# Optimization experiments

Measured on AMD Instinct MI355X. Metric: run time of the kernel, lower is better.

## Reference

```python
import jax, jax.numpy as jnp
import numpy as np

B, S, DIM, NH = 2, 2048, 1536, 12
HD = DIM // NH            # 128
C = HD // 2               # 64 rotary pairs
CF = C - 2 * (C // 3)     # 22 (frame axis)
CH = C // 3               # 21 (height axis)
CW = C // 3               # 21 (width axis)
GF, GH, GW = 8, 16, 16    # grid sizes, GF*GH*GW == S
EPS = 1e-6


def _freq_table(n_pos, dim):
    inv = 1.0 / (10000.0 ** (np.arange(dim, dtype=np.float64) / dim))
    ang = np.outer(np.arange(n_pos, dtype=np.float64), inv)
    return (np.cos(ang).astype(np.float32), np.sin(ang).astype(np.float32))


def setup_inputs() -> dict:
    key = jax.random.key(0)
    ks = jax.random.split(key, 8)
    scale = 0.02
    cos_f, sin_f = _freq_table(GF, CF)
    cos_h, sin_h = _freq_table(GH, CH)
    cos_w, sin_w = _freq_table(GW, CW)
    return {
        'x': jax.random.normal(ks[0], (B, S, DIM), dtype=jnp.float32),
        'seq_lens': jnp.array([2048, 1600], dtype=jnp.int32),
        'f': GF, 'h': GH, 'w': GW,
        'wq': scale * jax.random.normal(ks[1], (DIM, DIM), dtype=jnp.float32),
        'bq': jnp.zeros((DIM,), jnp.float32),
        'wk': scale * jax.random.normal(ks[2], (DIM, DIM), dtype=jnp.float32),
        'bk': jnp.zeros((DIM,), jnp.float32),
        'wv': scale * jax.random.normal(ks[3], (DIM, DIM), dtype=jnp.float32),
        'bv': jnp.zeros((DIM,), jnp.float32),
        'wo': scale * jax.random.normal(ks[4], (DIM, DIM), dtype=jnp.float32),
        'bo': jnp.zeros((DIM,), jnp.float32),
        'nq_w': jnp.ones((DIM,), jnp.float32),
        'nk_w': jnp.ones((DIM,), jnp.float32),
        'cos_f': jnp.asarray(cos_f), 'sin_f': jnp.asarray(sin_f),
        'cos_h': jnp.asarray(cos_h), 'sin_h': jnp.asarray(sin_h),
        'cos_w': jnp.asarray(cos_w), 'sin_w': jnp.asarray(sin_w),
    }


def _rmsnorm(t, wt):
    return t * jax.lax.rsqrt(jnp.mean(t * t, axis=-1, keepdims=True) + EPS) * wt


def _grid_rope(t, cos, sin, b, s):
    # t: [b, s, NH, HD] ; cos/sin: [s, 1, C] (per-position assembled freqs)
    tp = t.reshape(b, s, NH, C, 2)
    xr, xi = tp[..., 0], tp[..., 1]
    rr = xr * cos - xi * sin          # complex multiply by e^{i*theta}
    ri = xr * sin + xi * cos
    return jnp.stack([rr, ri], axis=-1).reshape(b, s, NH, HD)


def reference(x, seq_lens, f, h, w, wq, bq, wk, bk, wv, bv, wo, bo,
              nq_w, nk_w, cos_f, sin_f, cos_h, sin_h, cos_w, sin_w):
    b, s, _ = x.shape
    # QKV projections with RMSNorm on q/k over full dim (as in the module)
    q = _rmsnorm(x @ wq.T + bq, nq_w).reshape(b, s, NH, HD)
    k = _rmsnorm(x @ wk.T + bk, nk_w).reshape(b, s, NH, HD)
    v = (x @ wv.T + bv).reshape(b, s, NH, HD)
    # grid-indexed RoPE: zero offsets / target==grid => arange sampling per axis
    idx = jnp.arange(s)
    fi = idx // (h * w)
    hi = (idx // w) % h
    wi = idx % w
    cos = jnp.concatenate([cos_f[fi], cos_h[hi], cos_w[wi]], axis=-1)[:, None, :]
    sin = jnp.concatenate([sin_f[fi], sin_h[hi], sin_w[wi]], axis=-1)[:, None, :]
    qr = _grid_rope(q, cos, sin, b, s)
    kr = _grid_rope(k, cos, sin, b, s)
    # attention with ragged key-length masking (flash_attention k_lens)
    scale = 1.0 / jnp.sqrt(jnp.float32(HD))
    scores = jnp.einsum('bqnd,bknd->bnqk', qr, kr) * scale
    kmask = idx[None, :] < seq_lens[:, None]            # [b, s]
    scores = jnp.where(kmask[:, None, None, :], scores, jnp.float32(-1e30))
    attn = jax.nn.softmax(scores, axis=-1)
    out = jnp.einsum('bnqk,bknd->bqnd', attn, v).reshape(b, s, DIM)
    return out @ wo.T + bo
```

## Files before the change

kernel.cpp:

```cpp
#include <hip/hip_runtime.h>
#include <hip/hip_bf16.h>
#include <math.h>

#define DIM_  1536
#define NH_   12
#define HD_   128
#define S_    2048
#define B_    2
#define M_    (B_*S_)
#define WEL_  (DIM_*DIM_)

typedef __attribute__((ext_vector_type(8))) _Float16 f16x8;
typedef __attribute__((ext_vector_type(4))) short short4v;
typedef __attribute__((ext_vector_type(8))) short short8v;
typedef __attribute__((ext_vector_type(4))) float f32x4;

#define SSCALE_LOG2E (0.08838834764831845f * 1.4426950408889634f)

static __device__ __forceinline__ short f2h(float f) {
  union { _Float16 h; short s; } u;
  u.h = (_Float16)f;
  return u.s;
}

static __device__ __forceinline__ unsigned pk2h(float a, float b) {
  typedef __attribute__((ext_vector_type(2))) __fp16 fp16x2;
  union { fp16x2 v; unsigned u; } u2;
  u2.v = __builtin_amdgcn_cvt_pkrtz(a, b);
  return u2.u;
}

__global__ __launch_bounds__(256) void f2h5_k(
    const float* __restrict__ x, const float* __restrict__ wq,
    const float* __restrict__ wk, const float* __restrict__ wv,
    const float* __restrict__ wo,
    short* __restrict__ x16, short* __restrict__ w16, short* __restrict__ wo16)
{
  int i = blockIdx.x * 256 + threadIdx.x;
  const float* src; short* dst; int j;
  if (i < 786432)       { src = x;  dst = x16;            j = i; }
  else if (i < 1081344) { src = wq; dst = w16;            j = i - 786432; }
  else if (i < 1376256) { src = wk; dst = w16 + WEL_;     j = i - 1081344; }
  else if (i < 1671168) { src = wv; dst = w16 + 2 * WEL_; j = i - 1376256; }
  else                  { src = wo; dst = wo16;           j = i - 1671168; }
  const float4* p = (const float4*)src + (size_t)j * 2;
  float4 a = p[0], b = p[1];
  short8v o;
  o[0] = f2h(a.x); o[1] = f2h(a.y); o[2] = f2h(a.z); o[3] = f2h(a.w);
  o[4] = f2h(b.x); o[5] = f2h(b.y); o[6] = f2h(b.z); o[7] = f2h(b.w);
  *((short8v*)dst + j) = o;
}

template<int MODE>
static __device__ __forceinline__ void gemm16_core(
    const short* __restrict__ A16, const short* __restrict__ W16,
    const float* __restrict__ bias, short* __restrict__ Outp,
    int m0, int n0, char* __restrict__ Ab, char* __restrict__ Bb)
{
  const int tid = threadIdx.x;
  const int l  = tid & 63, w = tid >> 6;
  const int wr = w >> 1, wc = w & 1;
  const int lc = l & 15, lg = l >> 4;

  f32x4 acc[4][4] = {};

  const int rs  = w * 16 + (l >> 2);
  const int gsl = ((l & 3) ^ ((rs >> 1) & 3)) * 8;
  const short* gA0 = A16 + (size_t)(m0 + rs) * DIM_ + gsl;
  const short* gA1 = A16 + (size_t)(m0 + 64 + rs) * DIM_ + gsl;
  const short* gB0 = W16 + (size_t)(n0 + rs) * DIM_ + gsl;
  const short* gB1 = W16 + (size_t)(n0 + 64 + rs) * DIM_ + gsl;

#define GSTAGE(buf, k0)                                                        \
  {                                                                            \
    __builtin_amdgcn_global_load_lds(                                          \
        (const __attribute__((address_space(1))) unsigned*)(gA0 + (k0)),       \
        (__attribute__((address_space(3))) unsigned*)(Ab + (buf) * 8192 + w * 1024), 16, 0, 0); \
    __builtin_amdgcn_global_load_lds(                                          \
        (const __attribute__((address_space(1))) unsigned*)(gA1 + (k0)),       \
        (__attribute__((address_space(3))) unsigned*)(Ab + (buf) * 8192 + 4096 + w * 1024), 16, 0, 0); \
    __builtin_amdgcn_global_load_lds(                                          \
        (const __attribute__((address_space(1))) unsigned*)(gB0 + (k0)),       \
        (__attribute__((address_space(3))) unsigned*)(Bb + (buf) * 8192 + w * 1024), 16, 0, 0); \
    __builtin_amdgcn_global_load_lds(                                          \
        (const __attribute__((address_space(1))) unsigned*)(gB1 + (k0)),       \
        (__attribute__((address_space(3))) unsigned*)(Bb + (buf) * 8192 + 4096 + w * 1024), 16, 0, 0); \
  }

  GSTAGE(0, 0);
  __syncthreads();
  int cur = 0;
  for (int k0 = 0; k0 < DIM_; k0 += 32) {
    const char* Ac = Ab + cur * 8192;
    const char* Bc = Bb + cur * 8192;
    f16x8 af[4], bf[4];
#pragma unroll
    for (int mt = 0; mt < 4; ++mt) {
      int ar = wr * 64 + mt * 16 + lc;
      af[mt] = *(const f16x8*)(Ac + ar * 64 + ((lg ^ ((ar >> 1) & 3)) << 4));
    }
#pragma unroll
    for (int nt = 0; nt < 4; ++nt) {
      int br = wc * 64 + nt * 16 + lc;
      bf[nt] = *(const f16x8*)(Bc + br * 64 + ((lg ^ ((br >> 1) & 3)) << 4));
    }
    if (k0 + 32 < DIM_) GSTAGE(cur ^ 1, k0 + 32);
    __builtin_amdgcn_s_setprio(1);
#pragma unroll
    for (int mt = 0; mt < 4; ++mt)
#pragma unroll
      for (int nt = 0; nt < 4; ++nt)
        acc[mt][nt] = __builtin_amdgcn_mfma_f32_16x16x32_f16(af[mt], bf[nt], acc[mt][nt], 0, 0, 0);
    __builtin_amdgcn_s_setprio(0);
    __syncthreads();
    cur ^= 1;
  }
#undef GSTAGE

  if (MODE == 0) {
#pragma unroll
    for (int nt = 0; nt < 4; ++nt) {
      int col = n0 + wc * 64 + nt * 16 + lc;
      float bb = bias[col];
#pragma unroll
      for (int mt = 0; mt < 4; ++mt) {
#pragma unroll
        for (int r = 0; r < 4; ++r) {
          int rowm = m0 + wr * 64 + mt * 16 + lg * 4 + r;
          Outp[(size_t)rowm * DIM_ + col] = f2h(acc[mt][nt][r] + bb);
        }
      }
    }
  } else {
#pragma unroll
    for (int nt = 0; nt < 4; ++nt) {
      int colg = n0 + wc * 64 + nt * 16 + lc;
      int h = colg >> 7, d = colg & 127;
      float bb = bias[colg];
#pragma unroll
      for (int mt = 0; mt < 4; ++mt) {
        int rowg = m0 + wr * 64 + mt * 16 + lg * 4;
        int b = rowg >> 11, s = rowg & (S_ - 1);
        short4v o4;
#pragma unroll
        for (int r = 0; r < 4; ++r) o4[r] = f2h(acc[mt][nt][r] + bb);
        *(short4v*)(Outp + ((size_t)((b * NH_ + h) * HD_ + d)) * S_ + s) = o4;
      }
    }
  }
}

__global__ __launch_bounds__(256) void gemm_qkv16_k(
    const short* __restrict__ x16, const short* __restrict__ w16,
    const float* __restrict__ bq, const float* __restrict__ bk,
    const float* __restrict__ bv,
    short* __restrict__ q16, short* __restrict__ k16, short* __restrict__ vt)
{
  __shared__ __align__(16) char Ab[2][8192];
  __shared__ __align__(16) char Bb[2][8192];
  const int z = blockIdx.z;
  if (z == 2)
    gemm16_core<2>(x16, w16 + 2 * (size_t)WEL_, bv, vt,
                   blockIdx.y * 128, blockIdx.x * 128, &Ab[0][0], &Bb[0][0]);
  else
    gemm16_core<0>(x16, w16 + (size_t)z * WEL_, z ? bk : bq, z ? k16 : q16,
                   blockIdx.y * 128, blockIdx.x * 128, &Ab[0][0], &Bb[0][0]);
}

__global__ __launch_bounds__(256) void gemm_out64_k(
    const short* __restrict__ att16, const short* __restrict__ wo16,
    const float* __restrict__ bo, float* __restrict__ out)
{
  __shared__ __align__(16) char Ab[2][8192];
  __shared__ __align__(16) char Bb[2][4096];
  const int m0 = blockIdx.y * 128, n0 = blockIdx.x * 64;
  const int tid = threadIdx.x;
  const int l  = tid & 63, w = tid >> 6;
  const int lc = l & 15, lg = l >> 4;

  f32x4 acc[2][4] = {};

  const int rsA = w * 32 + (l >> 2);
  const int rsB = w * 16 + (l >> 2);
  const int gslA = ((l & 3) ^ ((rsA >> 1) & 3)) * 8;
  const int gslB = ((l & 3) ^ ((rsB >> 1) & 3)) * 8;
  const short* gA0 = att16 + (size_t)(m0 + rsA) * DIM_ + gslA;
  const short* gA1 = att16 + (size_t)(m0 + 16 + rsA) * DIM_ + gslA;
  const short* gB0 = wo16 + (size_t)(n0 + rsB) * DIM_ + gslB;

#define GSTAGE(buf, k0)                                                        \
  {                                                                            \
    __builtin_amdgcn_global_load_lds(                                          \
        (const __attribute__((address_space(1))) unsigned*)(gA0 + (k0)),       \
        (__attribute__((address_space(3))) unsigned*)(&Ab[buf][0] + w * 2048), 16, 0, 0); \
    __builtin_amdgcn_global_load_lds(                                          \
        (const __attribute__((address_space(1))) unsigned*)(gA1 + (k0)),       \
        (__attribute__((address_space(3))) unsigned*)(&Ab[buf][0] + w * 2048 + 1024), 16, 0, 0); \
    __builtin_amdgcn_global_load_lds(                                          \
        (const __attribute__((address_space(1))) unsigned*)(gB0 + (k0)),       \
        (__attribute__((address_space(3))) unsigned*)(&Bb[buf][0] + w * 1024), 16, 0, 0); \
  }

  GSTAGE(0, 0);
  __syncthreads();
  int cur = 0;
  for (int k0 = 0; k0 < DIM_; k0 += 32) {
    const char* Ac = &Ab[cur][0];
    const char* Bc = &Bb[cur][0];
    f16x8 af[2], bf[4];
#pragma unroll
    for (int mt = 0; mt < 2; ++mt) {
      int ar = w * 32 + mt * 16 + lc;
      af[mt] = *(const f16x8*)(Ac + ar * 64 + ((lg ^ ((ar >> 1) & 3)) << 4));
    }
#pragma unroll
    for (int nt = 0; nt < 4; ++nt) {
      int br = nt * 16 + lc;
      bf[nt] = *(const f16x8*)(Bc + br * 64 + ((lg ^ ((br >> 1) & 3)) << 4));
    }
    if (k0 + 32 < DIM_) GSTAGE(cur ^ 1, k0 + 32);
    __builtin_amdgcn_s_setprio(1);
#pragma unroll
    for (int mt = 0; mt < 2; ++mt)
#pragma unroll
      for (int nt = 0; nt < 4; ++nt)
        acc[mt][nt] = __builtin_amdgcn_mfma_f32_16x16x32_f16(af[mt], bf[nt], acc[mt][nt], 0, 0, 0);
    __builtin_amdgcn_s_setprio(0);
    __syncthreads();
    cur ^= 1;
  }
#undef GSTAGE

#pragma unroll
  for (int nt = 0; nt < 4; ++nt) {
    int col = n0 + nt * 16 + lc;
    float bb = bo[col];
#pragma unroll
    for (int mt = 0; mt < 2; ++mt) {
#pragma unroll
      for (int r = 0; r < 4; ++r) {
        int rowm = m0 + w * 32 + mt * 16 + lg * 4 + r;
        out[(size_t)rowm * DIM_ + col] = acc[mt][nt][r] + bb;
      }
    }
  }
}

__global__ __launch_bounds__(256) void rms_rope_pack16_k(
    const short* __restrict__ t, const float* __restrict__ w,
    const float* __restrict__ cf, const float* __restrict__ sf,
    const float* __restrict__ ch, const float* __restrict__ sh,
    const float* __restrict__ cw, const float* __restrict__ sw,
    short* __restrict__ outb, float qsc)
{
  const int row = blockIdx.x;
  const int b   = row >> 11;
  const int s   = row & (S_ - 1);
  const _Float16* rp = (const _Float16*)(t + (size_t)row * DIM_);

  float ss = 0.f;
  for (int i = threadIdx.x; i < DIM_; i += 256) {
    float v2 = (float)rp[i]; ss += v2 * v2;
  }
#pragma unroll
  for (int off = 32; off > 0; off >>= 1) ss += __shfl_down(ss, off);
  __shared__ float red[4];
  if ((threadIdx.x & 63) == 0) red[threadIdx.x >> 6] = ss;
  __syncthreads();
  float scale = rsqrtf((red[0] + red[1] + red[2] + red[3]) * (1.f / DIM_) + 1e-6f) * qsc;

  const int fi = s >> 8;
  const int hi = (s >> 4) & 15;
  const int wi = s & 15;

  for (int p = threadIdx.x; p < NH_ * 64; p += 256) {
    int n = p >> 6, c = p & 63;
    float co, si;
    if (c < 22)      { co = cf[fi * 22 + c];        si = sf[fi * 22 + c]; }
    else if (c < 43) { co = ch[hi * 21 + (c - 22)]; si = sh[hi * 21 + (c - 22)]; }
    else             { co = cw[wi * 21 + (c - 43)]; si = sw[wi * 21 + (c - 43)]; }
    int d0 = n * HD_ + 2 * c;
    float xr = (float)rp[d0]     * scale * w[d0];
    float xi = (float)rp[d0 + 1] * scale * w[d0 + 1];
    float rr = xr * co - xi * si;
    float ri = xr * si + xi * co;
    *(unsigned int*)(outb + (((size_t)(b * NH_ + n) * S_ + s) * HD_ + 2 * c)) = pk2h(rr, ri);
  }
}

__global__ __launch_bounds__(256) void attn_mfma5_k(
    const short* __restrict__ qb, const short* __restrict__ kb,
    const short* __restrict__ vtb, const int* __restrict__ seq_lens,
    short* __restrict__ o16)
{
  const int bh = blockIdx.y;
  const int b  = bh / NH_;
  const int h  = bh - b * NH_;
  const int q0 = blockIdx.x << 6;
  const int kvlen = seq_lens[b];
  const int tid  = threadIdx.x;
  const int wid  = tid >> 6;
  const int lane = tid & 63;
  const int lg   = lane >> 4;
  const int lc   = lane & 15;
  const int xo   = (lc & 7) << 4;

  __shared__ __align__(16) char Kt[16384];
  __shared__ __align__(16) char Vt[16384];
  __shared__ __align__(16) char Pt[4][2048];

  f16x8 bq[4];
  {
    const size_t base = ((size_t)bh * S_ + q0 + wid * 16 + lc) * HD_;
#pragma unroll
    for (int dc = 0; dc < 4; ++dc)
      bq[dc] = *(const f16x8*)(qb + base + dc * 32 + lg * 8);
  }

  const short* kgA = kb + ((size_t)bh * S_ + wid * 16 + lg) * HD_
                        + ((lc * 8) ^ (lg << 3));
  const short* kgB = kb + ((size_t)bh * S_ + wid * 16 + 4 + lg) * HD_
                        + ((lc * 8) ^ ((lg ^ 4) << 3));
  const short* vg  = vtb + ((size_t)bh * HD_ + wid * 32 + (lane >> 3)) * S_
                         + (((lane & 7) * 8) ^ ((lane >> 3) << 3));

#define STAGE_K()                                                              \
  {                                                                            \
    _Pragma("unroll")                                                          \
    for (int j = 0; j < 4; ++j) {                                              \
      const short* g = (j & 1) ? (kgB + ((j - 1) >> 1) * (8 * HD_))            \
                               : (kgA + (j >> 1) * (8 * HD_));                 \
      __builtin_amdgcn_global_load_lds(                                        \
          (const __attribute__((address_space(1))) unsigned*)g,                \
          (__attribute__((address_space(3))) unsigned*)(Kt + (wid * 16 + j * 4) * 256), \
          16, 0, 0);                                                           \
    }                                                                          \
  }
#define STAGE_V()                                                              \
  {                                                                            \
    _Pragma("unroll")                                                          \
    for (int j = 0; j < 4; ++j) {                                              \
      __builtin_amdgcn_global_load_lds(                                        \
          (const __attribute__((address_space(1))) unsigned*)(vg + j * 8 * S_),\
          (__attribute__((address_space(3))) unsigned*)(Vt + (wid * 32 + j * 8) * 128), \
          16, 0, 0);                                                           \
    }                                                                          \
  }

  f32x4 oacc[8] = {};
  float m = -3.0e38f, l = 0.f;

  const int nt = kvlen >> 6;

  STAGE_K();
  kgA += 64 * HD_; kgB += 64 * HD_;
  __syncthreads();

  for (int ti = 0; ti < nt; ++ti) {
    STAGE_V();
    vg += 64;

    f32x4 s[4];
    __builtin_amdgcn_s_setprio(1);
#pragma unroll
    for (int kt = 0; kt < 4; ++kt) {
      f32x4 a = {0.f, 0.f, 0.f, 0.f};
      const char* kr = Kt + (kt * 16 + lc) * 256;
#pragma unroll
      for (int dc = 0; dc < 4; ++dc) {
        f16x8 kf = *(const f16x8*)(kr + ((dc * 64 + lg * 16) ^ xo));
        a = __builtin_amdgcn_mfma_f32_16x16x32_f16(kf, bq[dc], a, 0, 0, 0);
      }
      s[kt] = a;
    }
    __builtin_amdgcn_s_setprio(0);

    float t0 = -3.0e38f;
#pragma unroll
    for (int kt = 0; kt < 4; ++kt)
#pragma unroll
      for (int r = 0; r < 4; ++r) t0 = fmaxf(t0, s[kt][r]);
    t0 = fmaxf(t0, __shfl_xor(t0, 16));
    t0 = fmaxf(t0, __shfl_xor(t0, 32));

    if (__any(t0 > m + 8.f)) {
      float mn = fmaxf(m, t0);
      float a  = exp2f(m - mn);
      m = mn; l *= a;
#pragma unroll
      for (int r = 0; r < 4; ++r) {
        float ar = __shfl(a, 4 * lg + r);
#pragma unroll
        for (int n = 0; n < 8; ++n) oacc[n][r] *= ar;
      }
    }
    float ls = 0.f;
#pragma unroll
    for (int kt = 0; kt < 4; ++kt)
#pragma unroll
      for (int r = 0; r < 4; ++r) {
        float p = exp2f(s[kt][r] - m); s[kt][r] = p; ls += p;
      }
    ls += __shfl_xor(ls, 16);
    ls += __shfl_xor(ls, 32);
    l += ls;

    {
      char* pr = Pt[wid] + lc * 128;
#pragma unroll
      for (int kt = 0; kt < 4; ++kt) {
#pragma unroll
        for (int rr = 0; rr < 2; ++rr) {
          unsigned u = pk2h(s[kt][2 * rr], s[kt][2 * rr + 1]);
          int off = (kt * 32 + lg * 8 + rr * 4) ^ xo;
          *(unsigned*)(pr + off) = u;
        }
      }
    }

    __syncthreads();

    if (ti + 1 < nt) {
      STAGE_K();
      kgA += 64 * HD_; kgB += 64 * HD_;
    }

    __builtin_amdgcn_s_setprio(1);
#pragma unroll
    for (int kc = 0; kc < 2; ++kc) {
      f16x8 pa = *(const f16x8*)(Pt[wid] + lc * 128 + ((kc * 64 + lg * 16) ^ xo));
#pragma unroll
      for (int n = 0; n < 8; ++n) {
        f16x8 vf = *(const f16x8*)(Vt + (n * 16 + lc) * 128 + ((kc * 64 + lg * 16) ^ xo));
        oacc[n] = __builtin_amdgcn_mfma_f32_16x16x32_f16(pa, vf, oacc[n], 0, 0, 0);
      }
    }
    __builtin_amdgcn_s_setprio(0);

    __syncthreads();
  }

#pragma unroll
  for (int r = 0; r < 4; ++r) {
    float li = 1.f / __shfl(l, 4 * lg + r);
    int qrow = q0 + wid * 16 + 4 * lg + r;
#pragma unroll
    for (int n = 0; n < 8; ++n)
      o16[((size_t)(b * S_ + qrow) * NH_ + h) * HD_ + n * 16 + lc] = f2h(oacc[n][r] * li);
  }
#undef STAGE_K
#undef STAGE_V
}

extern "C" void kernel_launch(void* const* d_in, const int* in_sizes, int n_in,
                              void* d_out, int out_size, void* d_ws, size_t ws_size,
                              hipStream_t stream) {
  const float* x        = (const float*)d_in[0];
  const int*   seq_lens = (const int*)d_in[1];
  const float* wq = (const float*)d_in[5];
  const float* bq = (const float*)d_in[6];
  const float* wk = (const float*)d_in[7];
  const float* bk = (const float*)d_in[8];
  const float* wv = (const float*)d_in[9];
  const float* bv = (const float*)d_in[10];
  const float* wo = (const float*)d_in[11];
  const float* bo = (const float*)d_in[12];
  const float* nq = (const float*)d_in[13];
  const float* nk = (const float*)d_in[14];
  const float* cf = (const float*)d_in[15];
  const float* sf = (const float*)d_in[16];
  const float* ch = (const float*)d_in[17];
  const float* sh = (const float*)d_in[18];
  const float* cw = (const float*)d_in[19];
  const float* sw = (const float*)d_in[20];

  const size_t rowelems = (size_t)M_ * DIM_;
  short* x16  = (short*)d_ws;
  short* w16  = x16 + rowelems;
  short* wo16 = w16 + 3 * (size_t)WEL_;
  short* q16  = wo16 + WEL_;
  short* k16  = q16 + rowelems;
  short* vt   = k16 + rowelems;
  short* qh   = vt + rowelems;
  short* kh   = qh + rowelems;
  short* att16 = q16;
  float* out = (float*)d_out;

  f2h5_k<<<7680, 256, 0, stream>>>(x, wq, wk, wv, wo, x16, w16, wo16);

  gemm_qkv16_k<<<dim3(DIM_ / 128, M_ / 128, 3), 256, 0, stream>>>(
      x16, w16, bq, bk, bv, q16, k16, vt);

  rms_rope_pack16_k<<<M_, 256, 0, stream>>>(q16, nq, cf, sf, ch, sh, cw, sw, qh,
                                            SSCALE_LOG2E);
  rms_rope_pack16_k<<<M_, 256, 0, stream>>>(k16, nk, cf, sf, ch, sh, cw, sw, kh, 1.0f);

  attn_mfma5_k<<<dim3(S_ / 64, B_ * NH_), 256, 0, stream>>>(qh, kh, vt, seq_lens, att16);

  gemm_out64_k<<<dim3(DIM_ / 64, M_ / 128), 256, 0, stream>>>(att16, wo16, bo, out);
}
```

Measured before the change: 248.8 us.

## Remap block IDs XCD-aware, issue prefetch earlier, merge q/k rms-rope launches

Flattens the grids of the QKV GEMM, attention and output GEMM kernels to 1D and remaps block IDs as (bid&7)*N + bid>>3. Consecutive blocks dispatched round-robin across the eight XCDs then receive contiguous work tiles, which should improve L2 reuse of shared A/B or K/V tiles. It also moves the global-to-LDS prefetch of the next K tile ahead of the LDS fragment reads to start memory traffic sooner. The two RMSNorm+RoPE launches are merged into one launch with a z dimension, saving one launch.

```diff
diff --git a/kernel.cpp b/kernel.cpp
--- a/kernel.cpp
+++ b/kernel.cpp
@@ -91,6 +91,7 @@
   __syncthreads();
   int cur = 0;
   for (int k0 = 0; k0 < DIM_; k0 += 32) {
+    if (k0 + 32 < DIM_) GSTAGE(cur ^ 1, k0 + 32);
     const char* Ac = Ab + cur * 8192;
     const char* Bc = Bb + cur * 8192;
     f16x8 af[4], bf[4];
@@ -104,7 +105,6 @@
       int br = wc * 64 + nt * 16 + lc;
       bf[nt] = *(const f16x8*)(Bc + br * 64 + ((lg ^ ((br >> 1) & 3)) << 4));
     }
-    if (k0 + 32 < DIM_) GSTAGE(cur ^ 1, k0 + 32);
     __builtin_amdgcn_s_setprio(1);
 #pragma unroll
     for (int mt = 0; mt < 4; ++mt)
@@ -158,13 +158,17 @@
 {
   __shared__ __align__(16) char Ab[2][8192];
   __shared__ __align__(16) char Bb[2][8192];
-  const int z = blockIdx.z;
+  const int bid = blockIdx.x;
+  const int wrk = (bid & 7) * 144 + (bid >> 3);
+  const int n   = wrk % 12;
+  const int m   = (wrk / 12) % 32;
+  const int z   = wrk / 384;
   if (z == 2)
     gemm16_core<2>(x16, w16 + 2 * (size_t)WEL_, bv, vt,
-                   blockIdx.y * 128, blockIdx.x * 128, &Ab[0][0], &Bb[0][0]);
+                   m * 128, n * 128, &Ab[0][0], &Bb[0][0]);
   else
     gemm16_core<0>(x16, w16 + (size_t)z * WEL_, z ? bk : bq, z ? k16 : q16,
-                   blockIdx.y * 128, blockIdx.x * 128, &Ab[0][0], &Bb[0][0]);
+                   m * 128, n * 128, &Ab[0][0], &Bb[0][0]);
 }
 
 __global__ __launch_bounds__(256) void gemm_out64_k(
@@ -173,7 +177,9 @@
 {
   __shared__ __align__(16) char Ab[2][8192];
   __shared__ __align__(16) char Bb[2][4096];
-  const int m0 = blockIdx.y * 128, n0 = blockIdx.x * 64;
+  const int bid = blockIdx.x;
+  const int wrk = (bid & 7) * 96 + (bid >> 3);
+  const int m0 = (wrk / 24) * 128, n0 = (wrk % 24) * 64;
   const int tid = threadIdx.x;
   const int l  = tid & 63, w = tid >> 6;
   const int lc = l & 15, lg = l >> 4;
@@ -205,6 +211,7 @@
   __syncthreads();
   int cur = 0;
   for (int k0 = 0; k0 < DIM_; k0 += 32) {
+    if (k0 + 32 < DIM_) GSTAGE(cur ^ 1, k0 + 32);
     const char* Ac = &Ab[cur][0];
     const char* Bc = &Bb[cur][0];
     f16x8 af[2], bf[4];
@@ -218,7 +225,6 @@
       int br = nt * 16 + lc;
       bf[nt] = *(const f16x8*)(Bc + br * 64 + ((lg ^ ((br >> 1) & 3)) << 4));
     }
-    if (k0 + 32 < DIM_) GSTAGE(cur ^ 1, k0 + 32);
     __builtin_amdgcn_s_setprio(1);
 #pragma unroll
     for (int mt = 0; mt < 2; ++mt)
@@ -246,13 +252,20 @@
   }
 }
 
-__global__ __launch_bounds__(256) void rms_rope_pack16_k(
-    const short* __restrict__ t, const float* __restrict__ w,
+__global__ __launch_bounds__(256) void rms_rope_qk_k(
+    const short* __restrict__ q16, const short* __restrict__ k16,
+    const float* __restrict__ nq, const float* __restrict__ nk,
     const float* __restrict__ cf, const float* __restrict__ sf,
     const float* __restrict__ ch, const float* __restrict__ sh,
     const float* __restrict__ cw, const float* __restrict__ sw,
-    short* __restrict__ outb, float qsc)
+    short* __restrict__ qh, short* __restrict__ kh)
 {
+  const int z   = blockIdx.y;
+  const short* t = z ? k16 : q16;
+  const float* w = z ? nk : nq;
+  short* outb   = z ? kh : qh;
+  const float qsc0 = z ? 1.0f : SSCALE_LOG2E;
+
   const int row = blockIdx.x;
   const int b   = row >> 11;
   const int s   = row & (S_ - 1);
@@ -267,7 +280,7 @@
   __shared__ float red[4];
   if ((threadIdx.x & 63) == 0) red[threadIdx.x >> 6] = ss;
   __syncthreads();
-  float scale = rsqrtf((red[0] + red[1] + red[2] + red[3]) * (1.f / DIM_) + 1e-6f) * qsc;
+  float scale = rsqrtf((red[0] + red[1] + red[2] + red[3]) * (1.f / DIM_) + 1e-6f) * qsc0;
 
   const int fi = s >> 8;
   const int hi = (s >> 4) & 15;
@@ -293,10 +306,12 @@
     const short* __restrict__ vtb, const int* __restrict__ seq_lens,
     short* __restrict__ o16)
 {
-  const int bh = blockIdx.y;
-  const int b  = bh / NH_;
-  const int h  = bh - b * NH_;
-  const int q0 = blockIdx.x << 6;
+  const int bid = blockIdx.x;
+  const int wrk = (bid & 7) * 96 + (bid >> 3);
+  const int bh  = wrk / 32;
+  const int b   = bh / NH_;
+  const int h   = bh - b * NH_;
+  const int q0  = (wrk % 32) << 6;
   const int kvlen = seq_lens[b];
   const int tid  = threadIdx.x;
   const int wid  = tid >> 6;
@@ -488,14 +503,12 @@
 
   f2h5_k<<<7680, 256, 0, stream>>>(x, wq, wk, wv, wo, x16, w16, wo16);
 
-  gemm_qkv16_k<<<dim3(DIM_ / 128, M_ / 128, 3), 256, 0, stream>>>(
-      x16, w16, bq, bk, bv, q16, k16, vt);
-
-  rms_rope_pack16_k<<<M_, 256, 0, stream>>>(q16, nq, cf, sf, ch, sh, cw, sw, qh,
-                                            SSCALE_LOG2E);
-  rms_rope_pack16_k<<<M_, 256, 0, stream>>>(k16, nk, cf, sf, ch, sh, cw, sw, kh, 1.0f);
-
-  attn_mfma5_k<<<dim3(S_ / 64, B_ * NH_), 256, 0, stream>>>(qh, kh, vt, seq_lens, att16);
-
-  gemm_out64_k<<<dim3(DIM_ / 64, M_ / 128), 256, 0, stream>>>(att16, wo16, bo, out);
-}
+  gemm_qkv16_k<<<1152, 256, 0, stream>>>(x16, w16, bq, bk, bv, q16, k16, vt);
+
+  rms_rope_qk_k<<<dim3(M_, 2), 256, 0, stream>>>(
+      q16, k16, nq, nk, cf, sf, ch, sh, cw, sw, qh, kh);
+
+  attn_mfma5_k<<<768, 256, 0, stream>>>(qh, kh, vt, seq_lens, att16);
+
+  gemm_out64_k<<<768, 256, 0, stream>>>(att16, wo16, bo, out);
+}
```

Result: slower. 267.1 us (+7.4%).
